# Optimization experiments

Measured on AMD Instinct MI355X. Metric: run time of the kernel, lower is better.

Reference implementation:

```python
import jax, jax.numpy as jnp
import numpy as np

B, H, L = 8, 256, 16384

def setup_inputs() -> dict:
    key = jax.random.key(0)
    k1, k2, k3 = jax.random.split(key, 3)
    u = jax.random.normal(k1, (B, H, L), dtype=jnp.float32)
    # SSM convolution kernel (H, L); small scale to keep tanh unsaturated
    k = jax.random.normal(k2, (H, L), dtype=jnp.float32) * 0.02
    # D feedthrough parameter (H, H); forward only uses its diagonal via einsum 'hh,bhl->bhl'
    D = jax.random.normal(k3, (H, H), dtype=jnp.float32)
    return {"u": u, "k": k, "D": D}

def reference(u, k, D):
    # circular FFT convolution: y = ifft(fft(u) * fft(k)).real
    u_s = jnp.fft.fft(u, axis=-1)          # (B,H,L) complex64
    k_s = jnp.fft.fft(k, axis=-1)          # (H,L)   complex64
    y = jnp.fft.ifft(u_s * k_s[None], axis=-1).real
    # D feedthrough: einsum 'hh,bhl->bhl' uses only diag(D)
    y = y + jnp.einsum('hh,bhl->bhl', D, u)
    return jnp.tanh(y)
```

## Files before the change

### kernel.cpp

```cpp
#include <hip/hip_runtime.h>
#include <math.h>

#define FFT_N 16384
#define NT 512
#define B_DIM 8
#define H_DIM 256

#define REGION 2048
#define RW (REGION + (REGION >> 5))
#define PAD(x) ((x) + ((x) >> 5))

#define WAVE_LDS_FENCE() do {                                   \
    __builtin_amdgcn_sched_barrier(0);                          \
    asm volatile("s_waitcnt lgkmcnt(0)" ::: "memory");          \
    __builtin_amdgcn_sched_barrier(0);                          \
} while (0)

__device__ __forceinline__ float2 cmul(float2 a, float2 b) {
    return make_float2(a.x * b.x - a.y * b.y, a.x * b.y + a.y * b.x);
}
__device__ __forceinline__ float2 cadd(float2 a, float2 b) { return make_float2(a.x + b.x, a.y + b.y); }
__device__ __forceinline__ float2 csub(float2 a, float2 b) { return make_float2(a.x - b.x, a.y - b.y); }
__device__ __forceinline__ float2 mulnegi(float2 z) { return make_float2(z.y, -z.x); }
__device__ __forceinline__ float2 mulposi(float2 z) { return make_float2(-z.y, z.x); }

__device__ __forceinline__ void bfly4(float2& a, float2& b, float2& c, float2& d,
                                      float2 w1, float2 w2, float2 w3) {
    float2 apc = cadd(a, c), amc = csub(a, c);
    float2 bpd = cadd(b, d), bmd = csub(b, d);
    float2 nib = mulnegi(bmd);
    a = cadd(apc, bpd);
    b = cmul(csub(apc, bpd), w2);
    c = cmul(cadd(amc, nib), w1);
    d = cmul(csub(amc, nib), w3);
}
__device__ __forceinline__ void bfly4_nw(float2& a, float2& b, float2& c, float2& d) {
    float2 apc = cadd(a, c), amc = csub(a, c);
    float2 bpd = cadd(b, d), bmd = csub(b, d);
    float2 nib = mulnegi(bmd);
    a = cadd(apc, bpd);
    b = csub(apc, bpd);
    c = cadd(amc, nib);
    d = csub(amc, nib);
}
__device__ __forceinline__ void ibfly4(float2& a, float2& b, float2& c, float2& d,
                                       float2 w1t, float2 w2t) {
    float2 w1 = make_float2(w1t.x, -w1t.y);
    float2 w2 = make_float2(w2t.x, -w2t.y);
    float2 bt = cmul(b, w2), dt = cmul(d, w2);
    float2 A = cadd(a, bt), Bb = csub(a, bt);
    float2 C = cadd(c, dt), Dd = csub(c, dt);
    float2 Cw = cmul(C, w1);
    float2 Dw = mulposi(cmul(Dd, w1));
    a = cadd(A, Cw);  c = csub(A, Cw);
    b = cadd(Bb, Dw); d = csub(Bb, Dw);
}
__device__ __forceinline__ void ibfly4_nw(float2& a, float2& b, float2& c, float2& d) {
    float2 A = cadd(a, b), Bb = csub(a, b);
    float2 C = cadd(c, d), Dd = csub(c, d);
    float2 Dw = mulposi(Dd);
    a = cadd(A, C);  c = csub(A, C);
    b = cadd(Bb, Dw); d = csub(Bb, Dw);
}

__device__ __forceinline__ void fwd_g01_half(float2 rh[16], const int t, const int par,
                                             const float2* __restrict__ tw) {
#pragma unroll
    for (int m0 = 0; m0 < 4; ++m0) {
        const int i = t + 512 * par + 1024 * m0;
        bfly4(rh[m0], rh[m0 + 4], rh[m0 + 8], rh[m0 + 12], tw[i], tw[2 * i], tw[3 * i]);
    }
    {
        const int ig = (t + 512 * par) * 4;
        const float2 w1 = tw[ig], w2 = tw[2 * ig], w3 = tw[3 * ig];
#pragma unroll
        for (int a = 0; a < 4; ++a)
            bfly4(rh[4 * a], rh[4 * a + 1], rh[4 * a + 2], rh[4 * a + 3], w1, w2, w3);
    }
}
__device__ __forceinline__ void inv_g01_half(float2 rh[16], const int t, const int par,
                                             const float2* __restrict__ tw) {
    {
        const int ig = (t + 512 * par) * 4;
        const float2 w1 = tw[ig], w2 = tw[2 * ig];
#pragma unroll
        for (int a = 0; a < 4; ++a)
            ibfly4(rh[4 * a], rh[4 * a + 1], rh[4 * a + 2], rh[4 * a + 3], w1, w2);
    }
#pragma unroll
    for (int m0 = 0; m0 < 4; ++m0) {
        const int i = t + 512 * par + 1024 * m0;
        ibfly4(rh[m0], rh[m0 + 4], rh[m0 + 8], rh[m0 + 12], tw[i], tw[2 * i]);
    }
}

__device__ __forceinline__ void fwd_mid_half(float2 rh[16], float* ldsx, float* ldsy,
                                             const int w, const int l, const int s,
                                             const float2* __restrict__ tw) {
#pragma unroll
    for (int jj = 0; jj < 16; ++jj) {
        const int a = w * RW + PAD(1024 * s + 64 * jj + l);
        rh[jj].x = ldsx[a]; rh[jj].y = ldsy[a];
    }
#pragma unroll
    for (int j0 = 0; j0 < 4; ++j0) {
        const int i1 = 1024 * j0 + 16 * l;
        bfly4(rh[j0], rh[j0 + 4], rh[j0 + 8], rh[j0 + 12], tw[i1], tw[2 * i1], tw[3 * i1]);
    }
    {
        const int i2 = 64 * l;
        const float2 w1 = tw[i2], w2 = tw[2 * i2], w3 = tw[3 * i2];
#pragma unroll
        for (int g = 0; g < 4; ++g)
            bfly4(rh[4 * g], rh[4 * g + 1], rh[4 * g + 2], rh[4 * g + 3], w1, w2, w3);
    }
#pragma unroll
    for (int jj = 0; jj < 16; ++jj) {
        const int a = w * RW + PAD(1024 * s + 64 * jj + l);
        ldsx[a] = rh[jj].x; ldsy[a] = rh[jj].y;
    }
    WAVE_LDS_FENCE();
    {
        const int lo = 64 * (l >> 2) + (l & 3);
#pragma unroll
        for (int jj = 0; jj < 16; ++jj) {
            const int a = w * RW + PAD(1024 * s + lo + 4 * jj);
            rh[jj].x = ldsx[a]; rh[jj].y = ldsy[a];
        }
    }
#pragma unroll
    for (int j0 = 0; j0 < 4; ++j0) {
        const int i3 = 1024 * j0 + 256 * (l & 3);
        bfly4(rh[j0], rh[j0 + 4], rh[j0 + 8], rh[j0 + 12], tw[i3], tw[2 * i3], tw[3 * i3]);
    }
    {
        const int i4 = 1024 * (l & 3);
        const float2 w1 = tw[i4], w2 = tw[2 * i4], w3 = tw[3 * i4];
#pragma unroll
        for (int g = 0; g < 4; ++g)
            bfly4(rh[4 * g], rh[4 * g + 1], rh[4 * g + 2], rh[4 * g + 3], w1, w2, w3);
    }
    {
        const int lo = 64 * (l >> 2) + (l & 3);
#pragma unroll
        for (int jj = 0; jj < 16; ++jj) {
            const int a = w * RW + PAD(1024 * s + lo + 4 * jj);
            ldsx[a] = rh[jj].x; ldsy[a] = rh[jj].y;
        }
    }
    WAVE_LDS_FENCE();
#pragma unroll
    for (int jj = 0; jj < 16; ++jj) {
        const int a = w * RW + PAD(1024 * s + 16 * l + jj);
        rh[jj].x = ldsx[a]; rh[jj].y = ldsy[a];
    }
#pragma unroll
    for (int g = 0; g < 4; ++g)
        bfly4_nw(rh[4 * g], rh[4 * g + 1], rh[4 * g + 2], rh[4 * g + 3]);
}
__device__ __forceinline__ void inv_mid_half(float2 rh[16], float* ldsx, float* ldsy,
                                             const int w, const int l, const int s,
                                             const float2* __restrict__ tw) {
#pragma unroll
    for (int g = 0; g < 4; ++g)
        ibfly4_nw(rh[4 * g], rh[4 * g + 1], rh[4 * g + 2], rh[4 * g + 3]);
#pragma unroll
    for (int jj = 0; jj < 16; ++jj) {
        const int a = w * RW + PAD(1024 * s + 16 * l + jj);
        ldsx[a] = rh[jj].x; ldsy[a] = rh[jj].y;
    }
    WAVE_LDS_FENCE();
    {
        const int lo = 64 * (l >> 2) + (l & 3);
#pragma unroll
        for (int jj = 0; jj < 16; ++jj) {
            const int a = w * RW + PAD(1024 * s + lo + 4 * jj);
            rh[jj].x = ldsx[a]; rh[jj].y = ldsy[a];
        }
    }
    {
        const int i4 = 1024 * (l & 3);
        const float2 w1 = tw[i4], w2 = tw[2 * i4];
#pragma unroll
        for (int g = 0; g < 4; ++g)
            ibfly4(rh[4 * g], rh[4 * g + 1], rh[4 * g + 2], rh[4 * g + 3], w1, w2);
    }
#pragma unroll
    for (int j0 = 0; j0 < 4; ++j0) {
        const int i3 = 1024 * j0 + 256 * (l & 3);
        ibfly4(rh[j0], rh[j0 + 4], rh[j0 + 8], rh[j0 + 12], tw[i3], tw[2 * i3]);
    }
    {
        const int lo = 64 * (l >> 2) + (l & 3);
#pragma unroll
        for (int jj = 0; jj < 16; ++jj) {
            const int a = w * RW + PAD(1024 * s + lo + 4 * jj);
            ldsx[a] = rh[jj].x; ldsy[a] = rh[jj].y;
        }
    }
    WAVE_LDS_FENCE();
#pragma unroll
    for (int jj = 0; jj < 16; ++jj) {
        const int a = w * RW + PAD(1024 * s + 64 * jj + l);
        rh[jj].x = ldsx[a]; rh[jj].y = ldsy[a];
    }
    {
        const int i2 = 64 * l;
        const float2 w1 = tw[i2], w2 = tw[2 * i2];
#pragma unroll
        for (int g = 0; g < 4; ++g)
            ibfly4(rh[4 * g], rh[4 * g + 1], rh[4 * g + 2], rh[4 * g + 3], w1, w2);
    }
#pragma unroll
    for (int j0 = 0; j0 < 4; ++j0) {
        const int i1 = 1024 * j0 + 16 * l;
        ibfly4(rh[j0], rh[j0 + 4], rh[j0 + 8], rh[j0 + 12], tw[i1], tw[2 * i1]);
    }
#pragma unroll
    for (int jj = 0; jj < 16; ++jj) {
        const int a = w * RW + PAD(1024 * s + 64 * jj + l);
        ldsx[a] = rh[jj].x; ldsy[a] = rh[jj].y;
    }
}

__device__ __forceinline__ float ftanh(float x) {
    float e = __expf(2.0f * x);
    return 1.0f - 2.0f * __builtin_amdgcn_rcpf(e + 1.0f);
}

__global__ void twiddle_init(float2* __restrict__ tw) {
    int t = blockIdx.x * blockDim.x + threadIdx.x;
    if (t < FFT_N) {
        float ang = -2.0f * 3.14159265358979323846f * (float)t / (float)FFT_N;
        float sv, cv;
        sincosf(ang, &sv, &cv);
        tw[t] = make_float2(cv, sv);
    }
}

__global__ __launch_bounds__(NT) void kfft_kernel(const float* __restrict__ k,
                                                  const float* __restrict__ D,
                                                  const float2* __restrict__ tw,
                                                  float2* __restrict__ Kf) {
    __shared__ float ldsx[8 * RW];
    __shared__ float ldsy[8 * RW];
    const int h = blockIdx.x;
    const int t = threadIdx.x;
    const int w = t >> 6, l = t & 63;
    const float* krow = k + (size_t)h * FFT_N;
    const float dh = D[h * (H_DIM + 1)];
#pragma unroll
    for (int par = 0; par < 2; ++par) {
        float2 rh[16];
#pragma unroll
        for (int m = 0; m < 16; ++m)
            rh[m] = make_float2(krow[t + 512 * par + 1024 * m], 0.f);
        if (par == 0 && t == 0) rh[0].x += dh;
        fwd_g01_half(rh, t, par, tw);
#pragma unroll
        for (int m = 0; m < 16; ++m) {
            const int e = t + 512 * par + 1024 * m;
            const int a = (e >> 11) * RW + PAD(e & 2047);
            ldsx[a] = rh[m].x; ldsy[a] = rh[m].y;
        }
    }
    __syncthreads();
    float4* out4 = (float4*)(Kf + (size_t)h * FFT_N);
#pragma unroll
    for (int s = 0; s < 2; ++s) {
        float2 rh[16];
        fwd_mid_half(rh, ldsx, ldsy, w, l, s, tw);
#pragma unroll
        for (int q = 0; q < 8; ++q)
            out4[16 * t + 8 * s + q] =
                make_float4(rh[2 * q].x, rh[2 * q].y, rh[2 * q + 1].x, rh[2 * q + 1].y);
    }
}

__global__ __launch_bounds__(NT) void conv_kernel(const float* __restrict__ u,
                                                  const float2* __restrict__ tw,
                                                  const float2* __restrict__ Kf,
                                                  float* __restrict__ out) {
    __shared__ float ldsx[8 * RW];
    __shared__ float ldsy[8 * RW];
    const int raw = blockIdx.x;
    const int vb = ((raw & 7) << 7) + (raw >> 3);
    const int h = vb >> 2;
    const int p = vb & 3;
    const int t = threadIdx.x;
    const int w = t >> 6, l = t & 63;
    const size_t row0 = ((size_t)(2 * p) * H_DIM + h) * FFT_N;
    const size_t row1 = row0 + (size_t)H_DIM * FFT_N;
    const float* u0 = u + row0;
    const float* u1 = u + row1;

#pragma unroll
    for (int par = 0; par < 2; ++par) {
        float2 rh[16];
#pragma unroll
        for (int m = 0; m < 16; ++m) {
            const int n = t + 512 * par + 1024 * m;
            rh[m] = make_float2(u0[n], u1[n]);
        }
        fwd_g01_half(rh, t, par, tw);
#pragma unroll
        for (int m = 0; m < 16; ++m) {
            const int e = t + 512 * par + 1024 * m;
            const int a = (e >> 11) * RW + PAD(e & 2047);
            ldsx[a] = rh[m].x; ldsy[a] = rh[m].y;
        }
    }
    __syncthreads();

    const float4* kf4 = (const float4*)(Kf + (size_t)h * FFT_N);
    const float invN = 1.0f / (float)FFT_N;
#pragma unroll
    for (int s = 0; s < 2; ++s) {
        float2 rh[16];
        fwd_mid_half(rh, ldsx, ldsy, w, l, s, tw);
#pragma unroll
        for (int q = 0; q < 8; ++q) {
            const float4 kw = kf4[16 * t + 8 * s + q];
            const float2 z0 = rh[2 * q], z1 = rh[2 * q + 1];
            rh[2 * q]     = make_float2((z0.x * kw.x - z0.y * kw.y) * invN,
                                        (z0.x * kw.y + z0.y * kw.x) * invN);
            rh[2 * q + 1] = make_float2((z1.x * kw.z - z1.y * kw.w) * invN,
                                        (z1.x * kw.w + z1.y * kw.z) * invN);
        }
        inv_mid_half(rh, ldsx, ldsy, w, l, s, tw);
    }
    __syncthreads();

    float* o0 = out + row0;
    float* o1 = out + row1;
#pragma unroll
    for (int par = 0; par < 2; ++par) {
        float2 rh[16];
#pragma unroll
        for (int m = 0; m < 16; ++m) {
            const int e = t + 512 * par + 1024 * m;
            const int a = (e >> 11) * RW + PAD(e & 2047);
            rh[m].x = ldsx[a]; rh[m].y = ldsy[a];
        }
        inv_g01_half(rh, t, par, tw);
#pragma unroll
        for (int m = 0; m < 16; ++m) {
            const int n = t + 512 * par + 1024 * m;
            o0[n] = ftanh(rh[m].x);
            o1[n] = ftanh(rh[m].y);
        }
    }
}

extern "C" void kernel_launch(void* const* d_in, const int* in_sizes, int n_in,
                              void* d_out, int out_size, void* d_ws, size_t ws_size,
                              hipStream_t stream) {
    const float* u = (const float*)d_in[0];
    const float* k = (const float*)d_in[1];
    const float* D = (const float*)d_in[2];
    float* out = (float*)d_out;

    float2* tw = (float2*)d_ws;
    float2* Kf = tw + FFT_N;

    twiddle_init<<<FFT_N / 256, 256, 0, stream>>>(tw);
    kfft_kernel<<<H_DIM, NT, 0, stream>>>(k, D, tw, Kf);
    conv_kernel<<<(B_DIM / 2) * H_DIM, NT, 0, stream>>>(u, tw, Kf, out);
}
```

Baseline: 224.1 us.

## Interleave the two sub-FFT halves per stage and fold 1/N into the kernel spectrum

The per-half mid-FFT helpers in conv_kernel are inlined and reordered so that each LDS exchange stage handles both s-halves before a single wave fence. This cuts the number of fences and gives the scheduler two independent halves to overlap LDS latency with butterflies. The 1/N normalisation moves into kfft_kernel's stored spectrum, which removes multiplies from the pointwise product. The Kf loads are also hoisted ahead of the LDS reads. The interleaving raises register pressure in the unrolled code.

```diff
diff --git a/kernel.cpp b/kernel.cpp
--- a/kernel.cpp
+++ b/kernel.cpp
@@ -158,70 +158,6 @@
     for (int g = 0; g < 4; ++g)
         bfly4_nw(rh[4 * g], rh[4 * g + 1], rh[4 * g + 2], rh[4 * g + 3]);
 }
-__device__ __forceinline__ void inv_mid_half(float2 rh[16], float* ldsx, float* ldsy,
-                                             const int w, const int l, const int s,
-                                             const float2* __restrict__ tw) {
-#pragma unroll
-    for (int g = 0; g < 4; ++g)
-        ibfly4_nw(rh[4 * g], rh[4 * g + 1], rh[4 * g + 2], rh[4 * g + 3]);
-#pragma unroll
-    for (int jj = 0; jj < 16; ++jj) {
-        const int a = w * RW + PAD(1024 * s + 16 * l + jj);
-        ldsx[a] = rh[jj].x; ldsy[a] = rh[jj].y;
-    }
-    WAVE_LDS_FENCE();
-    {
-        const int lo = 64 * (l >> 2) + (l & 3);
-#pragma unroll
-        for (int jj = 0; jj < 16; ++jj) {
-            const int a = w * RW + PAD(1024 * s + lo + 4 * jj);
-            rh[jj].x = ldsx[a]; rh[jj].y = ldsy[a];
-        }
-    }
-    {
-        const int i4 = 1024 * (l & 3);
-        const float2 w1 = tw[i4], w2 = tw[2 * i4];
-#pragma unroll
-        for (int g = 0; g < 4; ++g)
-            ibfly4(rh[4 * g], rh[4 * g + 1], rh[4 * g + 2], rh[4 * g + 3], w1, w2);
-    }
-#pragma unroll
-    for (int j0 = 0; j0 < 4; ++j0) {
-        const int i3 = 1024 * j0 + 256 * (l & 3);
-        ibfly4(rh[j0], rh[j0 + 4], rh[j0 + 8], rh[j0 + 12], tw[i3], tw[2 * i3]);
-    }
-    {
-        const int lo = 64 * (l >> 2) + (l & 3);
-#pragma unroll
-        for (int jj = 0; jj < 16; ++jj) {
-            const int a = w * RW + PAD(1024 * s + lo + 4 * jj);
-            ldsx[a] = rh[jj].x; ldsy[a] = rh[jj].y;
-        }
-    }
-    WAVE_LDS_FENCE();
-#pragma unroll
-    for (int jj = 0; jj < 16; ++jj) {
-        const int a = w * RW + PAD(1024 * s + 64 * jj + l);
-        rh[jj].x = ldsx[a]; rh[jj].y = ldsy[a];
-    }
-    {
-        const int i2 = 64 * l;
-        const float2 w1 = tw[i2], w2 = tw[2 * i2];
-#pragma unroll
-        for (int g = 0; g < 4; ++g)
-            ibfly4(rh[4 * g], rh[4 * g + 1], rh[4 * g + 2], rh[4 * g + 3], w1, w2);
-    }
-#pragma unroll
-    for (int j0 = 0; j0 < 4; ++j0) {
-        const int i1 = 1024 * j0 + 16 * l;
-        ibfly4(rh[j0], rh[j0 + 4], rh[j0 + 8], rh[j0 + 12], tw[i1], tw[2 * i1]);
-    }
-#pragma unroll
-    for (int jj = 0; jj < 16; ++jj) {
-        const int a = w * RW + PAD(1024 * s + 64 * jj + l);
-        ldsx[a] = rh[jj].x; ldsy[a] = rh[jj].y;
-    }
-}
 
 __device__ __forceinline__ float ftanh(float x) {
     float e = __expf(2.0f * x);
@@ -265,6 +201,7 @@
         }
     }
     __syncthreads();
+    const float invN = 1.0f / (float)FFT_N;
     float4* out4 = (float4*)(Kf + (size_t)h * FFT_N);
 #pragma unroll
     for (int s = 0; s < 2; ++s) {
@@ -273,7 +210,8 @@
 #pragma unroll
         for (int q = 0; q < 8; ++q)
             out4[16 * t + 8 * s + q] =
-                make_float4(rh[2 * q].x, rh[2 * q].y, rh[2 * q + 1].x, rh[2 * q + 1].y);
+                make_float4(rh[2 * q].x * invN, rh[2 * q].y * invN,
+                            rh[2 * q + 1].x * invN, rh[2 * q + 1].y * invN);
     }
 }
 
@@ -313,21 +251,152 @@
     __syncthreads();
 
     const float4* kf4 = (const float4*)(Kf + (size_t)h * FFT_N);
-    const float invN = 1.0f / (float)FFT_N;
-#pragma unroll
-    for (int s = 0; s < 2; ++s) {
-        float2 rh[16];
-        fwd_mid_half(rh, ldsx, ldsy, w, l, s, tw);
+    const int lo = 64 * (l >> 2) + (l & 3);
+
+#pragma unroll
+    for (int s = 0; s < 2; ++s) {
+        float2 rh[16];
+#pragma unroll
+        for (int jj = 0; jj < 16; ++jj) {
+            const int a = w * RW + PAD(1024 * s + 64 * jj + l);
+            rh[jj].x = ldsx[a]; rh[jj].y = ldsy[a];
+        }
+#pragma unroll
+        for (int j0 = 0; j0 < 4; ++j0) {
+            const int i1 = 1024 * j0 + 16 * l;
+            bfly4(rh[j0], rh[j0 + 4], rh[j0 + 8], rh[j0 + 12], tw[i1], tw[2 * i1], tw[3 * i1]);
+        }
+        {
+            const int i2 = 64 * l;
+            const float2 w1 = tw[i2], w2 = tw[2 * i2], w3 = tw[3 * i2];
+#pragma unroll
+            for (int g = 0; g < 4; ++g)
+                bfly4(rh[4 * g], rh[4 * g + 1], rh[4 * g + 2], rh[4 * g + 3], w1, w2, w3);
+        }
+#pragma unroll
+        for (int jj = 0; jj < 16; ++jj) {
+            const int a = w * RW + PAD(1024 * s + 64 * jj + l);
+            ldsx[a] = rh[jj].x; ldsy[a] = rh[jj].y;
+        }
+    }
+    WAVE_LDS_FENCE();
+
+#pragma unroll
+    for (int s = 0; s < 2; ++s) {
+        float2 rh[16];
+#pragma unroll
+        for (int jj = 0; jj < 16; ++jj) {
+            const int a = w * RW + PAD(1024 * s + lo + 4 * jj);
+            rh[jj].x = ldsx[a]; rh[jj].y = ldsy[a];
+        }
+#pragma unroll
+        for (int j0 = 0; j0 < 4; ++j0) {
+            const int i3 = 1024 * j0 + 256 * (l & 3);
+            bfly4(rh[j0], rh[j0 + 4], rh[j0 + 8], rh[j0 + 12], tw[i3], tw[2 * i3], tw[3 * i3]);
+        }
+        {
+            const int i4 = 1024 * (l & 3);
+            const float2 w1 = tw[i4], w2 = tw[2 * i4], w3 = tw[3 * i4];
+#pragma unroll
+            for (int g = 0; g < 4; ++g)
+                bfly4(rh[4 * g], rh[4 * g + 1], rh[4 * g + 2], rh[4 * g + 3], w1, w2, w3);
+        }
+#pragma unroll
+        for (int jj = 0; jj < 16; ++jj) {
+            const int a = w * RW + PAD(1024 * s + lo + 4 * jj);
+            ldsx[a] = rh[jj].x; ldsy[a] = rh[jj].y;
+        }
+    }
+    WAVE_LDS_FENCE();
+
+#pragma unroll
+    for (int s = 0; s < 2; ++s) {
+        float4 kq[8];
+#pragma unroll
+        for (int q = 0; q < 8; ++q) kq[q] = kf4[16 * t + 8 * s + q];
+        float2 rh[16];
+#pragma unroll
+        for (int jj = 0; jj < 16; ++jj) {
+            const int a = w * RW + PAD(1024 * s + 16 * l + jj);
+            rh[jj].x = ldsx[a]; rh[jj].y = ldsy[a];
+        }
+#pragma unroll
+        for (int g = 0; g < 4; ++g)
+            bfly4_nw(rh[4 * g], rh[4 * g + 1], rh[4 * g + 2], rh[4 * g + 3]);
 #pragma unroll
         for (int q = 0; q < 8; ++q) {
-            const float4 kw = kf4[16 * t + 8 * s + q];
-            const float2 z0 = rh[2 * q], z1 = rh[2 * q + 1];
-            rh[2 * q]     = make_float2((z0.x * kw.x - z0.y * kw.y) * invN,
-                                        (z0.x * kw.y + z0.y * kw.x) * invN);
-            rh[2 * q + 1] = make_float2((z1.x * kw.z - z1.y * kw.w) * invN,
-                                        (z1.x * kw.w + z1.y * kw.z) * invN);
-        }
-        inv_mid_half(rh, ldsx, ldsy, w, l, s, tw);
+            float2 z;
+            z = rh[2 * q];
+            rh[2 * q]     = make_float2(z.x * kq[q].x - z.y * kq[q].y,
+                                        z.x * kq[q].y + z.y * kq[q].x);
+            z = rh[2 * q + 1];
+            rh[2 * q + 1] = make_float2(z.x * kq[q].z - z.y * kq[q].w,
+                                        z.x * kq[q].w + z.y * kq[q].z);
+        }
+#pragma unroll
+        for (int g = 0; g < 4; ++g)
+            ibfly4_nw(rh[4 * g], rh[4 * g + 1], rh[4 * g + 2], rh[4 * g + 3]);
+#pragma unroll
+        for (int jj = 0; jj < 16; ++jj) {
+            const int a = w * RW + PAD(1024 * s + 16 * l + jj);
+            ldsx[a] = rh[jj].x; ldsy[a] = rh[jj].y;
+        }
+    }
+    WAVE_LDS_FENCE();
+
+#pragma unroll
+    for (int s = 0; s < 2; ++s) {
+        float2 rh[16];
+#pragma unroll
+        for (int jj = 0; jj < 16; ++jj) {
+            const int a = w * RW + PAD(1024 * s + lo + 4 * jj);
+            rh[jj].x = ldsx[a]; rh[jj].y = ldsy[a];
+        }
+        {
+            const int i4 = 1024 * (l & 3);
+            const float2 w1 = tw[i4], w2 = tw[2 * i4];
+#pragma unroll
+            for (int g = 0; g < 4; ++g)
+                ibfly4(rh[4 * g], rh[4 * g + 1], rh[4 * g + 2], rh[4 * g + 3], w1, w2);
+        }
+#pragma unroll
+        for (int j0 = 0; j0 < 4; ++j0) {
+            const int i3 = 1024 * j0 + 256 * (l & 3);
+            ibfly4(rh[j0], rh[j0 + 4], rh[j0 + 8], rh[j0 + 12], tw[i3], tw[2 * i3]);
+        }
+#pragma unroll
+        for (int jj = 0; jj < 16; ++jj) {
+            const int a = w * RW + PAD(1024 * s + lo + 4 * jj);
+            ldsx[a] = rh[jj].x; ldsy[a] = rh[jj].y;
+        }
+    }
+    WAVE_LDS_FENCE();
+
+#pragma unroll
+    for (int s = 0; s < 2; ++s) {
+        float2 rh[16];
+#pragma unroll
+        for (int jj = 0; jj < 16; ++jj) {
+            const int a = w * RW + PAD(1024 * s + 64 * jj + l);
+            rh[jj].x = ldsx[a]; rh[jj].y = ldsy[a];
+        }
+        {
+            const int i2 = 64 * l;
+            const float2 w1 = tw[i2], w2 = tw[2 * i2];
+#pragma unroll
+            for (int g = 0; g < 4; ++g)
+                ibfly4(rh[4 * g], rh[4 * g + 1], rh[4 * g + 2], rh[4 * g + 3], w1, w2);
+        }
+#pragma unroll
+        for (int j0 = 0; j0 < 4; ++j0) {
+            const int i1 = 1024 * j0 + 16 * l;
+            ibfly4(rh[j0], rh[j0 + 4], rh[j0 + 8], rh[j0 + 12], tw[i1], tw[2 * i1]);
+        }
+#pragma unroll
+        for (int jj = 0; jj < 16; ++jj) {
+            const int a = w * RW + PAD(1024 * s + 64 * jj + l);
+            ldsx[a] = rh[jj].x; ldsy[a] = rh[jj].y;
+        }
     }
     __syncthreads();
 
```

Result: faster. 216.0 us (-3.6%).

## Use 1024-thread blocks with swizzled interleaved float2 LDS for single-pass FFT

Applied to the files above, without the earlier changes.

Doubles the block size so each thread handles 16 points of the 16K FFT in one pass, instead of looping over two halves. The split, padded x/y LDS arrays become one interleaved float2 array with an XOR swizzle to avoid bank conflicts. The explicit per-wave LDS fences are dropped, and the 1/N scale is folded into the precomputed kernel spectrum. The aim is more resident waves for latency hiding and fewer LDS instructions, at the cost of a 128-VGPR budget per thread and 128KB of LDS per block.

```diff
diff --git a/kernel.cpp b/kernel.cpp
--- a/kernel.cpp
+++ b/kernel.cpp
@@ -2,19 +2,12 @@
 #include <math.h>
 
 #define FFT_N 16384
-#define NT 512
+#define NT 1024
 #define B_DIM 8
 #define H_DIM 256
 
-#define REGION 2048
-#define RW (REGION + (REGION >> 5))
-#define PAD(x) ((x) + ((x) >> 5))
-
-#define WAVE_LDS_FENCE() do {                                   \
-    __builtin_amdgcn_sched_barrier(0);                          \
-    asm volatile("s_waitcnt lgkmcnt(0)" ::: "memory");          \
-    __builtin_amdgcn_sched_barrier(0);                          \
-} while (0)
+#define SWZ2(a) ((a) ^ (((a) >> 5) & 15) ^ (((a) >> 9) & 1))
+
 
 __device__ __forceinline__ float2 cmul(float2 a, float2 b) {
     return make_float2(a.x * b.x - a.y * b.y, a.x * b.y + a.y * b.x);
@@ -63,163 +56,34 @@
     b = cadd(Bb, Dw); d = csub(Bb, Dw);
 }
 
-__device__ __forceinline__ void fwd_g01_half(float2 rh[16], const int t, const int par,
-                                             const float2* __restrict__ tw) {
+__device__ __forceinline__ void fwd_g01(float2 r[16], const int t,
+                                        const float2* __restrict__ tw) {
 #pragma unroll
     for (int m0 = 0; m0 < 4; ++m0) {
-        const int i = t + 512 * par + 1024 * m0;
-        bfly4(rh[m0], rh[m0 + 4], rh[m0 + 8], rh[m0 + 12], tw[i], tw[2 * i], tw[3 * i]);
-    }
-    {
-        const int ig = (t + 512 * par) * 4;
+        const int i = t + 1024 * m0;
+        bfly4(r[m0], r[m0 + 4], r[m0 + 8], r[m0 + 12], tw[i], tw[2 * i], tw[3 * i]);
+    }
+    {
+        const int ig = 4 * t;
         const float2 w1 = tw[ig], w2 = tw[2 * ig], w3 = tw[3 * ig];
 #pragma unroll
         for (int a = 0; a < 4; ++a)
-            bfly4(rh[4 * a], rh[4 * a + 1], rh[4 * a + 2], rh[4 * a + 3], w1, w2, w3);
-    }
-}
-__device__ __forceinline__ void inv_g01_half(float2 rh[16], const int t, const int par,
-                                             const float2* __restrict__ tw) {
-    {
-        const int ig = (t + 512 * par) * 4;
+            bfly4(r[4 * a], r[4 * a + 1], r[4 * a + 2], r[4 * a + 3], w1, w2, w3);
+    }
+}
+__device__ __forceinline__ void inv_g01(float2 r[16], const int t,
+                                        const float2* __restrict__ tw) {
+    {
+        const int ig = 4 * t;
         const float2 w1 = tw[ig], w2 = tw[2 * ig];
 #pragma unroll
         for (int a = 0; a < 4; ++a)
-            ibfly4(rh[4 * a], rh[4 * a + 1], rh[4 * a + 2], rh[4 * a + 3], w1, w2);
+            ibfly4(r[4 * a], r[4 * a + 1], r[4 * a + 2], r[4 * a + 3], w1, w2);
     }
 #pragma unroll
     for (int m0 = 0; m0 < 4; ++m0) {
-        const int i = t + 512 * par + 1024 * m0;
-        ibfly4(rh[m0], rh[m0 + 4], rh[m0 + 8], rh[m0 + 12], tw[i], tw[2 * i]);
-    }
-}
-
-__device__ __forceinline__ void fwd_mid_half(float2 rh[16], float* ldsx, float* ldsy,
-                                             const int w, const int l, const int s,
-                                             const float2* __restrict__ tw) {
-#pragma unroll
-    for (int jj = 0; jj < 16; ++jj) {
-        const int a = w * RW + PAD(1024 * s + 64 * jj + l);
-        rh[jj].x = ldsx[a]; rh[jj].y = ldsy[a];
-    }
-#pragma unroll
-    for (int j0 = 0; j0 < 4; ++j0) {
-        const int i1 = 1024 * j0 + 16 * l;
-        bfly4(rh[j0], rh[j0 + 4], rh[j0 + 8], rh[j0 + 12], tw[i1], tw[2 * i1], tw[3 * i1]);
-    }
-    {
-        const int i2 = 64 * l;
-        const float2 w1 = tw[i2], w2 = tw[2 * i2], w3 = tw[3 * i2];
-#pragma unroll
-        for (int g = 0; g < 4; ++g)
-            bfly4(rh[4 * g], rh[4 * g + 1], rh[4 * g + 2], rh[4 * g + 3], w1, w2, w3);
-    }
-#pragma unroll
-    for (int jj = 0; jj < 16; ++jj) {
-        const int a = w * RW + PAD(1024 * s + 64 * jj + l);
-        ldsx[a] = rh[jj].x; ldsy[a] = rh[jj].y;
-    }
-    WAVE_LDS_FENCE();
-    {
-        const int lo = 64 * (l >> 2) + (l & 3);
-#pragma unroll
-        for (int jj = 0; jj < 16; ++jj) {
-            const int a = w * RW + PAD(1024 * s + lo + 4 * jj);
-            rh[jj].x = ldsx[a]; rh[jj].y = ldsy[a];
-        }
-    }
-#pragma unroll
-    for (int j0 = 0; j0 < 4; ++j0) {
-        const int i3 = 1024 * j0 + 256 * (l & 3);
-        bfly4(rh[j0], rh[j0 + 4], rh[j0 + 8], rh[j0 + 12], tw[i3], tw[2 * i3], tw[3 * i3]);
-    }
-    {
-        const int i4 = 1024 * (l & 3);
-        const float2 w1 = tw[i4], w2 = tw[2 * i4], w3 = tw[3 * i4];
-#pragma unroll
-        for (int g = 0; g < 4; ++g)
-            bfly4(rh[4 * g], rh[4 * g + 1], rh[4 * g + 2], rh[4 * g + 3], w1, w2, w3);
-    }
-    {
-        const int lo = 64 * (l >> 2) + (l & 3);
-#pragma unroll
-        for (int jj = 0; jj < 16; ++jj) {
-            const int a = w * RW + PAD(1024 * s + lo + 4 * jj);
-            ldsx[a] = rh[jj].x; ldsy[a] = rh[jj].y;
-        }
-    }
-    WAVE_LDS_FENCE();
-#pragma unroll
-    for (int jj = 0; jj < 16; ++jj) {
-        const int a = w * RW + PAD(1024 * s + 16 * l + jj);
-        rh[jj].x = ldsx[a]; rh[jj].y = ldsy[a];
-    }
-#pragma unroll
-    for (int g = 0; g < 4; ++g)
-        bfly4_nw(rh[4 * g], rh[4 * g + 1], rh[4 * g + 2], rh[4 * g + 3]);
-}
-__device__ __forceinline__ void inv_mid_half(float2 rh[16], float* ldsx, float* ldsy,
-                                             const int w, const int l, const int s,
-                                             const float2* __restrict__ tw) {
-#pragma unroll
-    for (int g = 0; g < 4; ++g)
-        ibfly4_nw(rh[4 * g], rh[4 * g + 1], rh[4 * g + 2], rh[4 * g + 3]);
-#pragma unroll
-    for (int jj = 0; jj < 16; ++jj) {
-        const int a = w * RW + PAD(1024 * s + 16 * l + jj);
-        ldsx[a] = rh[jj].x; ldsy[a] = rh[jj].y;
-    }
-    WAVE_LDS_FENCE();
-    {
-        const int lo = 64 * (l >> 2) + (l & 3);
-#pragma unroll
-        for (int jj = 0; jj < 16; ++jj) {
-            const int a = w * RW + PAD(1024 * s + lo + 4 * jj);
-            rh[jj].x = ldsx[a]; rh[jj].y = ldsy[a];
-        }
-    }
-    {
-        const int i4 = 1024 * (l & 3);
-        const float2 w1 = tw[i4], w2 = tw[2 * i4];
-#pragma unroll
-        for (int g = 0; g < 4; ++g)
-            ibfly4(rh[4 * g], rh[4 * g + 1], rh[4 * g + 2], rh[4 * g + 3], w1, w2);
-    }
-#pragma unroll
-    for (int j0 = 0; j0 < 4; ++j0) {
-        const int i3 = 1024 * j0 + 256 * (l & 3);
-        ibfly4(rh[j0], rh[j0 + 4], rh[j0 + 8], rh[j0 + 12], tw[i3], tw[2 * i3]);
-    }
-    {
-        const int lo = 64 * (l >> 2) + (l & 3);
-#pragma unroll
-        for (int jj = 0; jj < 16; ++jj) {
-            const int a = w * RW + PAD(1024 * s + lo + 4 * jj);
-            ldsx[a] = rh[jj].x; ldsy[a] = rh[jj].y;
-        }
-    }
-    WAVE_LDS_FENCE();
-#pragma unroll
-    for (int jj = 0; jj < 16; ++jj) {
-        const int a = w * RW + PAD(1024 * s + 64 * jj + l);
-        rh[jj].x = ldsx[a]; rh[jj].y = ldsy[a];
-    }
-    {
-        const int i2 = 64 * l;
-        const float2 w1 = tw[i2], w2 = tw[2 * i2];
-#pragma unroll
-        for (int g = 0; g < 4; ++g)
-            ibfly4(rh[4 * g], rh[4 * g + 1], rh[4 * g + 2], rh[4 * g + 3], w1, w2);
-    }
-#pragma unroll
-    for (int j0 = 0; j0 < 4; ++j0) {
-        const int i1 = 1024 * j0 + 16 * l;
-        ibfly4(rh[j0], rh[j0 + 4], rh[j0 + 8], rh[j0 + 12], tw[i1], tw[2 * i1]);
-    }
-#pragma unroll
-    for (int jj = 0; jj < 16; ++jj) {
-        const int a = w * RW + PAD(1024 * s + 64 * jj + l);
-        ldsx[a] = rh[jj].x; ldsy[a] = rh[jj].y;
+        const int i = t + 1024 * m0;
+        ibfly4(r[m0], r[m0 + 4], r[m0 + 8], r[m0 + 12], tw[i], tw[2 * i]);
     }
 }
 
@@ -242,113 +106,201 @@
                                                   const float* __restrict__ D,
                                                   const float2* __restrict__ tw,
                                                   float2* __restrict__ Kf) {
-    __shared__ float ldsx[8 * RW];
-    __shared__ float ldsy[8 * RW];
+    __shared__ float2 lds2[FFT_N];
     const int h = blockIdx.x;
     const int t = threadIdx.x;
     const int w = t >> 6, l = t & 63;
+    const int base = 1024 * w;
+    const int lo = 64 * (l >> 2) + (l & 3);
     const float* krow = k + (size_t)h * FFT_N;
-    const float dh = D[h * (H_DIM + 1)];
-#pragma unroll
-    for (int par = 0; par < 2; ++par) {
-        float2 rh[16];
-#pragma unroll
-        for (int m = 0; m < 16; ++m)
-            rh[m] = make_float2(krow[t + 512 * par + 1024 * m], 0.f);
-        if (par == 0 && t == 0) rh[0].x += dh;
-        fwd_g01_half(rh, t, par, tw);
-#pragma unroll
-        for (int m = 0; m < 16; ++m) {
-            const int e = t + 512 * par + 1024 * m;
-            const int a = (e >> 11) * RW + PAD(e & 2047);
-            ldsx[a] = rh[m].x; ldsy[a] = rh[m].y;
-        }
-    }
+
+    float2 r[16];
+#pragma unroll
+    for (int m = 0; m < 16; ++m) r[m] = make_float2(krow[t + 1024 * m], 0.f);
+    if (t == 0) r[0].x += D[h * (H_DIM + 1)];
+    fwd_g01(r, t, tw);
+#pragma unroll
+    for (int m = 0; m < 16; ++m) lds2[SWZ2(t + 1024 * m)] = r[m];
     __syncthreads();
+
+#pragma unroll
+    for (int jj = 0; jj < 16; ++jj) r[jj] = lds2[SWZ2(base + 64 * jj + l)];
+#pragma unroll
+    for (int j0 = 0; j0 < 4; ++j0) {
+        const int i1 = 1024 * j0 + 16 * l;
+        bfly4(r[j0], r[j0 + 4], r[j0 + 8], r[j0 + 12], tw[i1], tw[2 * i1], tw[3 * i1]);
+    }
+    {
+        const int i2 = 64 * l;
+        const float2 w1 = tw[i2], w2 = tw[2 * i2], w3 = tw[3 * i2];
+#pragma unroll
+        for (int g = 0; g < 4; ++g)
+            bfly4(r[4 * g], r[4 * g + 1], r[4 * g + 2], r[4 * g + 3], w1, w2, w3);
+    }
+#pragma unroll
+    for (int jj = 0; jj < 16; ++jj) lds2[SWZ2(base + 64 * jj + l)] = r[jj];
+
+#pragma unroll
+    for (int jj = 0; jj < 16; ++jj) r[jj] = lds2[SWZ2(base + lo + 4 * jj)];
+#pragma unroll
+    for (int j0 = 0; j0 < 4; ++j0) {
+        const int i3 = 1024 * j0 + 256 * (l & 3);
+        bfly4(r[j0], r[j0 + 4], r[j0 + 8], r[j0 + 12], tw[i3], tw[2 * i3], tw[3 * i3]);
+    }
+    {
+        const int i4 = 1024 * (l & 3);
+        const float2 w1 = tw[i4], w2 = tw[2 * i4], w3 = tw[3 * i4];
+#pragma unroll
+        for (int g = 0; g < 4; ++g)
+            bfly4(r[4 * g], r[4 * g + 1], r[4 * g + 2], r[4 * g + 3], w1, w2, w3);
+    }
+#pragma unroll
+    for (int jj = 0; jj < 16; ++jj) lds2[SWZ2(base + lo + 4 * jj)] = r[jj];
+
+#pragma unroll
+    for (int jj = 0; jj < 16; ++jj) r[jj] = lds2[SWZ2(base + 16 * l + jj)];
+#pragma unroll
+    for (int g = 0; g < 4; ++g)
+        bfly4_nw(r[4 * g], r[4 * g + 1], r[4 * g + 2], r[4 * g + 3]);
+    const float invN = 1.0f / (float)FFT_N;
     float4* out4 = (float4*)(Kf + (size_t)h * FFT_N);
 #pragma unroll
-    for (int s = 0; s < 2; ++s) {
-        float2 rh[16];
-        fwd_mid_half(rh, ldsx, ldsy, w, l, s, tw);
-#pragma unroll
-        for (int q = 0; q < 8; ++q)
-            out4[16 * t + 8 * s + q] =
-                make_float4(rh[2 * q].x, rh[2 * q].y, rh[2 * q + 1].x, rh[2 * q + 1].y);
-    }
+    for (int q = 0; q < 8; ++q)
+        out4[8 * t + q] = make_float4(r[2 * q].x * invN, r[2 * q].y * invN,
+                                      r[2 * q + 1].x * invN, r[2 * q + 1].y * invN);
 }
 
 __global__ __launch_bounds__(NT) void conv_kernel(const float* __restrict__ u,
                                                   const float2* __restrict__ tw,
                                                   const float2* __restrict__ Kf,
                                                   float* __restrict__ out) {
-    __shared__ float ldsx[8 * RW];
-    __shared__ float ldsy[8 * RW];
+    __shared__ float2 lds2[FFT_N];
     const int raw = blockIdx.x;
     const int vb = ((raw & 7) << 7) + (raw >> 3);
     const int h = vb >> 2;
     const int p = vb & 3;
     const int t = threadIdx.x;
     const int w = t >> 6, l = t & 63;
+    const int base = 1024 * w;
+    const int lo = 64 * (l >> 2) + (l & 3);
     const size_t row0 = ((size_t)(2 * p) * H_DIM + h) * FFT_N;
     const size_t row1 = row0 + (size_t)H_DIM * FFT_N;
     const float* u0 = u + row0;
     const float* u1 = u + row1;
 
-#pragma unroll
-    for (int par = 0; par < 2; ++par) {
-        float2 rh[16];
-#pragma unroll
-        for (int m = 0; m < 16; ++m) {
-            const int n = t + 512 * par + 1024 * m;
-            rh[m] = make_float2(u0[n], u1[n]);
+    float2 r[16];
+#pragma unroll
+    for (int m = 0; m < 16; ++m) {
+        const int e = t + 1024 * m;
+        r[m] = make_float2(u0[e], u1[e]);
+    }
+    fwd_g01(r, t, tw);
+#pragma unroll
+    for (int m = 0; m < 16; ++m) lds2[SWZ2(t + 1024 * m)] = r[m];
+    __syncthreads();
+
+#pragma unroll
+    for (int jj = 0; jj < 16; ++jj) r[jj] = lds2[SWZ2(base + 64 * jj + l)];
+#pragma unroll
+    for (int j0 = 0; j0 < 4; ++j0) {
+        const int i1 = 1024 * j0 + 16 * l;
+        bfly4(r[j0], r[j0 + 4], r[j0 + 8], r[j0 + 12], tw[i1], tw[2 * i1], tw[3 * i1]);
+    }
+    {
+        const int i2 = 64 * l;
+        const float2 w1 = tw[i2], w2 = tw[2 * i2], w3 = tw[3 * i2];
+#pragma unroll
+        for (int g = 0; g < 4; ++g)
+            bfly4(r[4 * g], r[4 * g + 1], r[4 * g + 2], r[4 * g + 3], w1, w2, w3);
+    }
+#pragma unroll
+    for (int jj = 0; jj < 16; ++jj) lds2[SWZ2(base + 64 * jj + l)] = r[jj];
+
+#pragma unroll
+    for (int jj = 0; jj < 16; ++jj) r[jj] = lds2[SWZ2(base + lo + 4 * jj)];
+#pragma unroll
+    for (int j0 = 0; j0 < 4; ++j0) {
+        const int i3 = 1024 * j0 + 256 * (l & 3);
+        bfly4(r[j0], r[j0 + 4], r[j0 + 8], r[j0 + 12], tw[i3], tw[2 * i3], tw[3 * i3]);
+    }
+    {
+        const int i4 = 1024 * (l & 3);
+        const float2 w1 = tw[i4], w2 = tw[2 * i4], w3 = tw[3 * i4];
+#pragma unroll
+        for (int g = 0; g < 4; ++g)
+            bfly4(r[4 * g], r[4 * g + 1], r[4 * g + 2], r[4 * g + 3], w1, w2, w3);
+    }
+#pragma unroll
+    for (int jj = 0; jj < 16; ++jj) lds2[SWZ2(base + lo + 4 * jj)] = r[jj];
+
+#pragma unroll
+    for (int jj = 0; jj < 16; ++jj) r[jj] = lds2[SWZ2(base + 16 * l + jj)];
+#pragma unroll
+    for (int g = 0; g < 4; ++g)
+        bfly4_nw(r[4 * g], r[4 * g + 1], r[4 * g + 2], r[4 * g + 3]);
+    {
+        const float4* kf4 = (const float4*)(Kf + (size_t)h * FFT_N);
+#pragma unroll
+        for (int q = 0; q < 8; ++q) {
+            const float4 kq = kf4[8 * t + q];
+            float2 z;
+            z = r[2 * q];
+            r[2 * q]     = make_float2(z.x * kq.x - z.y * kq.y, z.x * kq.y + z.y * kq.x);
+            z = r[2 * q + 1];
+            r[2 * q + 1] = make_float2(z.x * kq.z - z.y * kq.w, z.x * kq.w + z.y * kq.z);
         }
-        fwd_g01_half(rh, t, par, tw);
-#pragma unroll
-        for (int m = 0; m < 16; ++m) {
-            const int e = t + 512 * par + 1024 * m;
-            const int a = (e >> 11) * RW + PAD(e & 2047);
-            ldsx[a] = rh[m].x; ldsy[a] = rh[m].y;
-        }
-    }
+    }
+#pragma unroll
+    for (int g = 0; g < 4; ++g)
+        ibfly4_nw(r[4 * g], r[4 * g + 1], r[4 * g + 2], r[4 * g + 3]);
+#pragma unroll
+    for (int jj = 0; jj < 16; ++jj) lds2[SWZ2(base + 16 * l + jj)] = r[jj];
+
+#pragma unroll
+    for (int jj = 0; jj < 16; ++jj) r[jj] = lds2[SWZ2(base + lo + 4 * jj)];
+    {
+        const int i4 = 1024 * (l & 3);
+        const float2 w1 = tw[i4], w2 = tw[2 * i4];
+#pragma unroll
+        for (int g = 0; g < 4; ++g)
+            ibfly4(r[4 * g], r[4 * g + 1], r[4 * g + 2], r[4 * g + 3], w1, w2);
+    }
+#pragma unroll
+    for (int j0 = 0; j0 < 4; ++j0) {
+        const int i3 = 1024 * j0 + 256 * (l & 3);
+        ibfly4(r[j0], r[j0 + 4], r[j0 + 8], r[j0 + 12], tw[i3], tw[2 * i3]);
+    }
+#pragma unroll
+    for (int jj = 0; jj < 16; ++jj) lds2[SWZ2(base + lo + 4 * jj)] = r[jj];
+
+#pragma unroll
+    for (int jj = 0; jj < 16; ++jj) r[jj] = lds2[SWZ2(base + 64 * jj + l)];
+    {
+        const int i2 = 64 * l;
+        const float2 w1 = tw[i2], w2 = tw[2 * i2];
+#pragma unroll
+        for (int g = 0; g < 4; ++g)
+            ibfly4(r[4 * g], r[4 * g + 1], r[4 * g + 2], r[4 * g + 3], w1, w2);
+    }
+#pragma unroll
+    for (int j0 = 0; j0 < 4; ++j0) {
+        const int i1 = 1024 * j0 + 16 * l;
+        ibfly4(r[j0], r[j0 + 4], r[j0 + 8], r[j0 + 12], tw[i1], tw[2 * i1]);
+    }
+#pragma unroll
+    for (int jj = 0; jj < 16; ++jj) lds2[SWZ2(base + 64 * jj + l)] = r[jj];
     __syncthreads();
 
-    const float4* kf4 = (const float4*)(Kf + (size_t)h * FFT_N);
-    const float invN = 1.0f / (float)FFT_N;
-#pragma unroll
-    for (int s = 0; s < 2; ++s) {
-        float2 rh[16];
-        fwd_mid_half(rh, ldsx, ldsy, w, l, s, tw);
-#pragma unroll
-        for (int q = 0; q < 8; ++q) {
-            const float4 kw = kf4[16 * t + 8 * s + q];
-            const float2 z0 = rh[2 * q], z1 = rh[2 * q + 1];
-            rh[2 * q]     = make_float2((z0.x * kw.x - z0.y * kw.y) * invN,
-                                        (z0.x * kw.y + z0.y * kw.x) * invN);
-            rh[2 * q + 1] = make_float2((z1.x * kw.z - z1.y * kw.w) * invN,
-                                        (z1.x * kw.w + z1.y * kw.z) * invN);
-        }
-        inv_mid_half(rh, ldsx, ldsy, w, l, s, tw);
-    }
-    __syncthreads();
-
+#pragma unroll
+    for (int m = 0; m < 16; ++m) r[m] = lds2[SWZ2(t + 1024 * m)];
+    inv_g01(r, t, tw);
     float* o0 = out + row0;
     float* o1 = out + row1;
 #pragma unroll
-    for (int par = 0; par < 2; ++par) {
-        float2 rh[16];
-#pragma unroll
-        for (int m = 0; m < 16; ++m) {
-            const int e = t + 512 * par + 1024 * m;
-            const int a = (e >> 11) * RW + PAD(e & 2047);
-            rh[m].x = ldsx[a]; rh[m].y = ldsy[a];
-        }
-        inv_g01_half(rh, t, par, tw);
-#pragma unroll
-        for (int m = 0; m < 16; ++m) {
-            const int n = t + 512 * par + 1024 * m;
-            o0[n] = ftanh(rh[m].x);
-            o1[n] = ftanh(rh[m].y);
-        }
+    for (int m = 0; m < 16; ++m) {
+        const int e = t + 1024 * m;
+        o0[e] = ftanh(r[m].x);
+        o1[e] = ftanh(r[m].y);
     }
 }
 
```

Result: slower. 263.3 us (+17.5%).
